# Optimization experiments

Hardware: AMD Instinct MI355X
Metric: run time of the kernel (lower is better)

Reference implementation:

```python
import jax, jax.numpy as jnp
import numpy as np

HIDDEN = 128
N_H = 32
E = 262144


def setup_inputs() -> dict:
    key = jax.random.key(0)
    ks = jax.random.split(key, 10)
    s = lambda fan_in: 1.0 / np.sqrt(fan_in)
    return {
        "h_i": jax.random.normal(ks[0], (E, N_H), dtype=jnp.float32),
        "e_ij": jax.random.normal(ks[1], (E, 1), dtype=jnp.float32),
        # lin_A1: 1 -> HIDDEN
        "W_A1": jax.random.uniform(ks[2], (1, HIDDEN), jnp.float32, -s(1), s(1)),
        "b_A1": jnp.zeros((HIDDEN,), jnp.float32),
        # lin_A2: HIDDEN -> N_H*N_H
        "W_A2": jax.random.uniform(ks[3], (HIDDEN, N_H * N_H), jnp.float32, -s(HIDDEN), s(HIDDEN)),
        "b_A2": jnp.zeros((N_H * N_H,), jnp.float32),
        # lin_b1: 1 -> HIDDEN
        "W_b1": jax.random.uniform(ks[4], (1, HIDDEN), jnp.float32, -s(1), s(1)),
        "b_b1": jnp.zeros((HIDDEN,), jnp.float32),
        # lin_b2: HIDDEN -> N_H
        "W_b2": jax.random.uniform(ks[5], (HIDDEN, N_H), jnp.float32, -s(HIDDEN), s(HIDDEN)),
        "b_b2": jnp.zeros((N_H,), jnp.float32),
    }


def reference(h_i, e_ij, W_A1, b_A1, W_A2, b_A2, W_b1, b_b1, W_b2, b_b2):
    # Per-edge MLP producing an [N_H, N_H] matrix A from the scalar edge feature
    A = jax.nn.selu(e_ij @ W_A1 + b_A1)          # [E, HIDDEN]
    A = (A @ W_A2 + b_A2).reshape(-1, N_H, N_H)  # [E, N_H, N_H]
    # Per-edge MLP producing an [N_H] bias b
    b = jax.nn.selu(e_ij @ W_b1 + b_b1)          # [E, HIDDEN]
    b = b @ W_b2 + b_b2                          # [E, N_H]
    # Batched matvec: m_ij[e, i] = sum_j A[e, i, j] * h_i[e, j] + b[e, i]
    m_ij = jnp.einsum('eij,ej->ei', A, h_i) + b
    return m_ij
```

## Files before the change

kernel.cpp:

```cpp
#include <hip/hip_runtime.h>

#define NH        32
#define HID       128
#define E_TOT     262144
#define CH_ELEM   16384
#define NCH_MAIN  8
#define TAIL_OFF  131072
#define TAIL_ELEM 8192

typedef float        f32x4 __attribute__((ext_vector_type(4)));
typedef short        s16x8 __attribute__((ext_vector_type(8)));
typedef unsigned int u32x4 __attribute__((ext_vector_type(4)));

static __device__ __forceinline__ short f2bf(float f) {
    __bf16 b = (__bf16)f;
    return __builtin_bit_cast(short, b);
}
static __device__ __forceinline__ float selu_f(float x) {
    const float kScale  = 1.0507009873554804934193349852946f;
    const float kAlphaS = 1.7580993408473768599402175208123f;
    float neg = kAlphaS * (__expf(x) - 1.0f);
    return x > 0.0f ? kScale * x : neg;
}

__global__ void wt_build(const float* __restrict__ W_A2, const float* __restrict__ b_A2,
                         const float* __restrict__ W_b2, unsigned short* __restrict__ WT) {
    int gid = blockIdx.x * 256 + threadIdx.x;
    if (gid >= TAIL_OFF + TAIL_ELEM) return;
    int it, g, lrow, p, kap;
    if (gid < TAIL_OFF) {
        int c  = gid >> 14;
        int r  = gid & 16383;
        int sl = r >> 10;
        it   = (r >> 9) & 1;
        g    = (r >> 7) & 3;
        lrow = (r >> 3) & 15;
        p    = r & 7;
        kap  = c * 512 + sl * 32 + g * 8 + p;
    } else {
        int r  = gid - TAIL_OFF;
        int sl = r >> 10;
        it   = (r >> 9) & 1;
        g    = (r >> 7) & 3;
        lrow = (r >> 3) & 15;
        p    = r & 7;
        kap  = 4096 + sl * 32 + g * 8 + p;
    }
    int i = it * 16 + lrow;
    float v = 0.0f;
    if (kap < 4096)      v = W_A2[(kap >> 5) * 1024 + i * 32 + (kap & 31)];
    else if (kap < 4128) v = b_A2[i * 32 + (kap - 4096)];
    else if (kap < 4256) v = W_b2[(kap - 4128) * 32 + i];
    WT[gid] = (unsigned short)f2bf(v);
}

typedef const __attribute__((address_space(1))) unsigned int GU32;
typedef __attribute__((address_space(3))) unsigned int LU32;
static __device__ __forceinline__ void gload_lds16(const void* g, void* l) {
    __builtin_amdgcn_global_load_lds((GU32*)g, (LU32*)l, 16, 0, 0);
}

__global__ void __launch_bounds__(256, 4)
msg_main(const float* __restrict__ h_i, const float* __restrict__ e_ij,
         const float* __restrict__ W_A1, const float* __restrict__ b_A1,
         const float* __restrict__ W_b1, const float* __restrict__ b_b1,
         const float* __restrict__ b_b2,
         const unsigned short* __restrict__ WT,
         float* __restrict__ out)
{
    __shared__ unsigned short ldsW[CH_ELEM];
    __shared__ float cA1[HID], cBA1[HID], cB1a[HID], cB1b[HID], cb2[NH];

    const int tid  = threadIdx.x;
    const int lane = tid & 63;
    const int wid  = tid >> 6;
    const int lrow = lane & 15;
    const int g    = lane >> 4;
    const int e0   = blockIdx.x * 256 + wid * 64;

    if (tid < HID) {
        cA1[tid]  = W_A1[tid];
        cBA1[tid] = b_A1[tid];
        cB1a[tid] = W_b1[tid];
        cB1b[tid] = b_b1[tid];
    }
    if (tid < NH) cb2[tid] = b_b2[tid];

    const float ev_own = e_ij[e0 + lane];

    s16x8 hb[4];
    #pragma unroll
    for (int ct = 0; ct < 4; ++ct) {
        int er = e0 + ct * 16 + lrow;
        const float* hp = h_i + er * 32 + g * 8;
        f32x4 h0 = *(const f32x4*)hp;
        f32x4 h1 = *(const f32x4*)(hp + 4);
        #pragma unroll
        for (int p = 0; p < 4; ++p) {
            hb[ct][p]     = f2bf(h0[p]);
            hb[ct][p + 4] = f2bf(h1[p]);
        }
    }

    float ev_ct[4];
    #pragma unroll
    for (int ct = 0; ct < 4; ++ct) ev_ct[ct] = __shfl(ev_own, ct * 16 + lrow);

    f32x4 acc[4][2];
    #pragma unroll
    for (int ct = 0; ct < 4; ++ct)
        #pragma unroll
        for (int it = 0; it < 2; ++it)
            acc[ct][it] = (f32x4){0.f, 0.f, 0.f, 0.f};
    const f32x4 zf = (f32x4){0.f, 0.f, 0.f, 0.f};

    float u_own[16];

    __syncthreads();

    for (int c = 0; c < NCH_MAIN; ++c) {
        #pragma unroll
        for (int r = 0; r < 8; ++r) {
            int eo = r * 2048 + tid * 8;
            gload_lds16(WT + c * CH_ELEM + eo, &ldsW[eo]);
        }
        #pragma unroll
        for (int sl = 0; sl < 16; ++sl) {
            int s = c * 16 + sl;
            u_own[sl] = selu_f(fmaf(ev_own, cA1[s], cBA1[s]));
        }
        __syncthreads();

        #pragma unroll
        for (int sl = 0; sl < 16; ++sl) {
            u32x4 r0 = *(const u32x4*)&ldsW[sl * 1024 +       lane * 8];
            u32x4 r1 = *(const u32x4*)&ldsW[sl * 1024 + 512 + lane * 8];
            s16x8 A0 = __builtin_bit_cast(s16x8, r0);
            s16x8 A1 = __builtin_bit_cast(s16x8, r1);
            f32x4 u4[4];
            #pragma unroll
            for (int ct = 0; ct < 4; ++ct) {
                float uv = __shfl(u_own[sl], ct * 16 + lrow);
                u4[ct] = (f32x4){uv, uv, uv, uv};
            }
            {
                f32x4 t[4];
                #pragma unroll
                for (int ct = 0; ct < 4; ++ct)
                    t[ct] = __builtin_amdgcn_mfma_f32_16x16x32_bf16(A0, hb[ct], zf, 0, 0, 0);
                #pragma unroll
                for (int ct = 0; ct < 4; ++ct)
                    acc[ct][0] = __builtin_elementwise_fma(t[ct], u4[ct], acc[ct][0]);
            }
            {
                f32x4 t[4];
                #pragma unroll
                for (int ct = 0; ct < 4; ++ct)
                    t[ct] = __builtin_amdgcn_mfma_f32_16x16x32_bf16(A1, hb[ct], zf, 0, 0, 0);
                #pragma unroll
                for (int ct = 0; ct < 4; ++ct)
                    acc[ct][1] = __builtin_elementwise_fma(t[ct], u4[ct], acc[ct][1]);
            }
        }
        __syncthreads();
    }

    #pragma unroll
    for (int r = 0; r < 3; ++r) {
        int eo = r * 2048 + tid * 8;
        gload_lds16(WT + TAIL_OFF + eo, &ldsW[eo]);
    }
    __syncthreads();

    {
        u32x4 r0 = *(const u32x4*)&ldsW[      lane * 8];
        u32x4 r1 = *(const u32x4*)&ldsW[512 + lane * 8];
        s16x8 A0 = __builtin_bit_cast(s16x8, r0);
        s16x8 A1 = __builtin_bit_cast(s16x8, r1);
        #pragma unroll
        for (int ct = 0; ct < 4; ++ct) {
            acc[ct][0] = __builtin_amdgcn_mfma_f32_16x16x32_bf16(A0, hb[ct], acc[ct][0], 0, 0, 0);
            acc[ct][1] = __builtin_amdgcn_mfma_f32_16x16x32_bf16(A1, hb[ct], acc[ct][1], 0, 0, 0);
        }
    }
    #pragma unroll
    for (int q = 0; q < 4; ++q) {
        u32x4 r0 = *(const u32x4*)&ldsW[(q + 1) * 1024 +       lane * 8];
        u32x4 r1 = *(const u32x4*)&ldsW[(q + 1) * 1024 + 512 + lane * 8];
        s16x8 A0 = __builtin_bit_cast(s16x8, r0);
        s16x8 A1 = __builtin_bit_cast(s16x8, r1);
        int tb = q * 32 + g * 8;
        f32x4 wb0 = *(const f32x4*)&cB1a[tb];
        f32x4 wb1 = *(const f32x4*)&cB1a[tb + 4];
        f32x4 bb0 = *(const f32x4*)&cB1b[tb];
        f32x4 bb1 = *(const f32x4*)&cB1b[tb + 4];
        #pragma unroll
        for (int ct = 0; ct < 4; ++ct) {
            s16x8 B;
            #pragma unroll
            for (int p = 0; p < 4; ++p) {
                B[p]     = f2bf(selu_f(fmaf(ev_ct[ct], wb0[p], bb0[p])));
                B[p + 4] = f2bf(selu_f(fmaf(ev_ct[ct], wb1[p], bb1[p])));
            }
            acc[ct][0] = __builtin_amdgcn_mfma_f32_16x16x32_bf16(A0, B, acc[ct][0], 0, 0, 0);
            acc[ct][1] = __builtin_amdgcn_mfma_f32_16x16x32_bf16(A1, B, acc[ct][1], 0, 0, 0);
        }
    }

    #pragma unroll
    for (int it = 0; it < 2; ++it) {
        f32x4 b2v = *(const f32x4*)&cb2[it * 16 + g * 4];
        #pragma unroll
        for (int ct = 0; ct < 4; ++ct) {
            int edge = e0 + ct * 16 + lrow;
            f32x4 vo = acc[ct][it] + b2v;
            *(f32x4*)&out[edge * 32 + it * 16 + g * 4] = vo;
        }
    }
}

extern "C" void kernel_launch(void* const* d_in, const int* in_sizes, int n_in,
                              void* d_out, int out_size, void* d_ws, size_t ws_size,
                              hipStream_t stream) {
    const float* h_i  = (const float*)d_in[0];
    const float* e_ij = (const float*)d_in[1];
    const float* W_A1 = (const float*)d_in[2];
    const float* b_A1 = (const float*)d_in[3];
    const float* W_A2 = (const float*)d_in[4];
    const float* b_A2 = (const float*)d_in[5];
    const float* W_b1 = (const float*)d_in[6];
    const float* b_b1 = (const float*)d_in[7];
    const float* W_b2 = (const float*)d_in[8];
    const float* b_b2 = (const float*)d_in[9];

    unsigned short* WT = (unsigned short*)d_ws;

    wt_build<<<(TAIL_OFF + TAIL_ELEM + 255) / 256, 256, 0, stream>>>(W_A2, b_A2, W_b2, WT);
    msg_main<<<E_TOT / 256, 256, 0, stream>>>(h_i, e_ij, W_A1, b_A1, W_b1, b_b1,
                                              b_b2, WT, (float*)d_out);
}
```

Measured before the change: 97.62 us.

## Split output rows across wave pairs with 512-thread blocks

Each block now runs 8 waves instead of 4. Each pair of waves shares the same 64 edges, and each wave computes one half (16 rows) of the 32-row output. This halves the accumulator registers and MFMA work per wave and raises wave-level parallelism, but each wave now redundantly loads h, computes the selu hidden units and does the b-path selu. The hidden activations are also packed as bf16 pairs, which halves the shuffle count but makes the scale factors coarser than the fp32 values used before.

```diff
diff --git a/kernel.cpp b/kernel.cpp
--- a/kernel.cpp
+++ b/kernel.cpp
@@ -27,12 +27,12 @@
                          const float* __restrict__ W_b2, unsigned short* __restrict__ WT) {
     int gid = blockIdx.x * 256 + threadIdx.x;
     if (gid >= TAIL_OFF + TAIL_ELEM) return;
-    int it, g, lrow, p, kap;
+    int ih, g, lrow, p, kap;
     if (gid < TAIL_OFF) {
         int c  = gid >> 14;
         int r  = gid & 16383;
         int sl = r >> 10;
-        it   = (r >> 9) & 1;
+        ih   = (r >> 9) & 1;
         g    = (r >> 7) & 3;
         lrow = (r >> 3) & 15;
         p    = r & 7;
@@ -40,13 +40,13 @@
     } else {
         int r  = gid - TAIL_OFF;
         int sl = r >> 10;
-        it   = (r >> 9) & 1;
+        ih   = (r >> 9) & 1;
         g    = (r >> 7) & 3;
         lrow = (r >> 3) & 15;
         p    = r & 7;
         kap  = 4096 + sl * 32 + g * 8 + p;
     }
-    int i = it * 16 + lrow;
+    int i = ih * 16 + lrow;
     float v = 0.0f;
     if (kap < 4096)      v = W_A2[(kap >> 5) * 1024 + i * 32 + (kap & 31)];
     else if (kap < 4128) v = b_A2[i * 32 + (kap - 4096)];
@@ -60,7 +60,7 @@
     __builtin_amdgcn_global_load_lds((GU32*)g, (LU32*)l, 16, 0, 0);
 }
 
-__global__ void __launch_bounds__(256, 4)
+__global__ void __launch_bounds__(512, 4)
 msg_main(const float* __restrict__ h_i, const float* __restrict__ e_ij,
          const float* __restrict__ W_A1, const float* __restrict__ b_A1,
          const float* __restrict__ W_b1, const float* __restrict__ b_b1,
@@ -74,9 +74,11 @@
     const int tid  = threadIdx.x;
     const int lane = tid & 63;
     const int wid  = tid >> 6;
+    const int ih   = wid & 1;
+    const int eg   = wid >> 1;
     const int lrow = lane & 15;
     const int g    = lane >> 4;
-    const int e0   = blockIdx.x * 256 + wid * 64;
+    const int e0   = blockIdx.x * 256 + eg * 64;
 
     if (tid < HID) {
         cA1[tid]  = W_A1[tid];
@@ -106,89 +108,80 @@
     #pragma unroll
     for (int ct = 0; ct < 4; ++ct) ev_ct[ct] = __shfl(ev_own, ct * 16 + lrow);
 
-    f32x4 acc[4][2];
-    #pragma unroll
-    for (int ct = 0; ct < 4; ++ct)
-        #pragma unroll
-        for (int it = 0; it < 2; ++it)
-            acc[ct][it] = (f32x4){0.f, 0.f, 0.f, 0.f};
+    f32x4 acc[4];
+    #pragma unroll
+    for (int ct = 0; ct < 4; ++ct) acc[ct] = (f32x4){0.f, 0.f, 0.f, 0.f};
     const f32x4 zf = (f32x4){0.f, 0.f, 0.f, 0.f};
 
-    float u_own[16];
+    unsigned int u_pk[8];
 
     __syncthreads();
 
     for (int c = 0; c < NCH_MAIN; ++c) {
         #pragma unroll
-        for (int r = 0; r < 8; ++r) {
-            int eo = r * 2048 + tid * 8;
+        for (int r = 0; r < 4; ++r) {
+            int eo = r * 4096 + tid * 8;
             gload_lds16(WT + c * CH_ELEM + eo, &ldsW[eo]);
         }
         #pragma unroll
-        for (int sl = 0; sl < 16; ++sl) {
-            int s = c * 16 + sl;
-            u_own[sl] = selu_f(fmaf(ev_own, cA1[s], cBA1[s]));
+        for (int sp = 0; sp < 8; ++sp) {
+            int s = c * 16 + sp * 2;
+            float u0 = selu_f(fmaf(ev_own, cA1[s],     cBA1[s]));
+            float u1 = selu_f(fmaf(ev_own, cA1[s + 1], cBA1[s + 1]));
+            u_pk[sp] = ((unsigned int)(unsigned short)f2bf(u0))
+                     | (((unsigned int)(unsigned short)f2bf(u1)) << 16);
         }
         __syncthreads();
 
         #pragma unroll
-        for (int sl = 0; sl < 16; ++sl) {
-            u32x4 r0 = *(const u32x4*)&ldsW[sl * 1024 +       lane * 8];
-            u32x4 r1 = *(const u32x4*)&ldsW[sl * 1024 + 512 + lane * 8];
-            s16x8 A0 = __builtin_bit_cast(s16x8, r0);
-            s16x8 A1 = __builtin_bit_cast(s16x8, r1);
-            f32x4 u4[4];
+        for (int sp = 0; sp < 8; ++sp) {
+            unsigned int upc[4];
             #pragma unroll
-            for (int ct = 0; ct < 4; ++ct) {
-                float uv = __shfl(u_own[sl], ct * 16 + lrow);
-                u4[ct] = (f32x4){uv, uv, uv, uv};
-            }
-            {
+            for (int ct = 0; ct < 4; ++ct)
+                upc[ct] = __shfl(u_pk[sp], ct * 16 + lrow);
+
+            #pragma unroll
+            for (int half = 0; half < 2; ++half) {
+                const int sl = sp * 2 + half;
+                u32x4 ra = *(const u32x4*)&ldsW[sl * 1024 + ih * 512 + lane * 8];
+                s16x8 A  = __builtin_bit_cast(s16x8, ra);
+                f32x4 u4[4];
+                #pragma unroll
+                for (int ct = 0; ct < 4; ++ct) {
+                    unsigned int w = half == 0 ? (upc[ct] << 16) : (upc[ct] & 0xffff0000u);
+                    float uf = __builtin_bit_cast(float, w);
+                    u4[ct] = (f32x4){uf, uf, uf, uf};
+                }
                 f32x4 t[4];
                 #pragma unroll
                 for (int ct = 0; ct < 4; ++ct)
-                    t[ct] = __builtin_amdgcn_mfma_f32_16x16x32_bf16(A0, hb[ct], zf, 0, 0, 0);
+                    t[ct] = __builtin_amdgcn_mfma_f32_16x16x32_bf16(A, hb[ct], zf, 0, 0, 0);
                 #pragma unroll
                 for (int ct = 0; ct < 4; ++ct)
-                    acc[ct][0] = __builtin_elementwise_fma(t[ct], u4[ct], acc[ct][0]);
+                    acc[ct] = __builtin_elementwise_fma(t[ct], u4[ct], acc[ct]);
             }
-            {
-                f32x4 t[4];
-                #pragma unroll
-                for (int ct = 0; ct < 4; ++ct)
-                    t[ct] = __builtin_amdgcn_mfma_f32_16x16x32_bf16(A1, hb[ct], zf, 0, 0, 0);
-                #pragma unroll
-                for (int ct = 0; ct < 4; ++ct)
-                    acc[ct][1] = __builtin_elementwise_fma(t[ct], u4[ct], acc[ct][1]);
-            }
         }
         __syncthreads();
     }
 
     #pragma unroll
-    for (int r = 0; r < 3; ++r) {
-        int eo = r * 2048 + tid * 8;
+    for (int r = 0; r < 2; ++r) {
+        int eo = r * 4096 + tid * 8;
         gload_lds16(WT + TAIL_OFF + eo, &ldsW[eo]);
     }
     __syncthreads();
 
     {
-        u32x4 r0 = *(const u32x4*)&ldsW[      lane * 8];
-        u32x4 r1 = *(const u32x4*)&ldsW[512 + lane * 8];
-        s16x8 A0 = __builtin_bit_cast(s16x8, r0);
-        s16x8 A1 = __builtin_bit_cast(s16x8, r1);
-        #pragma unroll
-        for (int ct = 0; ct < 4; ++ct) {
-            acc[ct][0] = __builtin_amdgcn_mfma_f32_16x16x32_bf16(A0, hb[ct], acc[ct][0], 0, 0, 0);
-            acc[ct][1] = __builtin_amdgcn_mfma_f32_16x16x32_bf16(A1, hb[ct], acc[ct][1], 0, 0, 0);
-        }
+        u32x4 ra = *(const u32x4*)&ldsW[ih * 512 + lane * 8];
+        s16x8 A  = __builtin_bit_cast(s16x8, ra);
+        #pragma unroll
+        for (int ct = 0; ct < 4; ++ct)
+            acc[ct] = __builtin_amdgcn_mfma_f32_16x16x32_bf16(A, hb[ct], acc[ct], 0, 0, 0);
     }
     #pragma unroll
     for (int q = 0; q < 4; ++q) {
-        u32x4 r0 = *(const u32x4*)&ldsW[(q + 1) * 1024 +       lane * 8];
-        u32x4 r1 = *(const u32x4*)&ldsW[(q + 1) * 1024 + 512 + lane * 8];
-        s16x8 A0 = __builtin_bit_cast(s16x8, r0);
-        s16x8 A1 = __builtin_bit_cast(s16x8, r1);
+        u32x4 ra = *(const u32x4*)&ldsW[(q + 1) * 1024 + ih * 512 + lane * 8];
+        s16x8 A  = __builtin_bit_cast(s16x8, ra);
         int tb = q * 32 + g * 8;
         f32x4 wb0 = *(const f32x4*)&cB1a[tb];
         f32x4 wb1 = *(const f32x4*)&cB1a[tb + 4];
@@ -202,19 +195,17 @@
                 B[p]     = f2bf(selu_f(fmaf(ev_ct[ct], wb0[p], bb0[p])));
                 B[p + 4] = f2bf(selu_f(fmaf(ev_ct[ct], wb1[p], bb1[p])));
             }
-            acc[ct][0] = __builtin_amdgcn_mfma_f32_16x16x32_bf16(A0, B, acc[ct][0], 0, 0, 0);
-            acc[ct][1] = __builtin_amdgcn_mfma_f32_16x16x32_bf16(A1, B, acc[ct][1], 0, 0, 0);
-        }
-    }
-
-    #pragma unroll
-    for (int it = 0; it < 2; ++it) {
-        f32x4 b2v = *(const f32x4*)&cb2[it * 16 + g * 4];
+            acc[ct] = __builtin_amdgcn_mfma_f32_16x16x32_bf16(A, B, acc[ct], 0, 0, 0);
+        }
+    }
+
+    {
+        f32x4 b2v = *(const f32x4*)&cb2[ih * 16 + g * 4];
         #pragma unroll
         for (int ct = 0; ct < 4; ++ct) {
             int edge = e0 + ct * 16 + lrow;
-            f32x4 vo = acc[ct][it] + b2v;
-            *(f32x4*)&out[edge * 32 + it * 16 + g * 4] = vo;
+            f32x4 vo = acc[ct] + b2v;
+            *(f32x4*)&out[edge * 32 + ih * 16 + g * 4] = vo;
         }
     }
 }
@@ -236,6 +227,6 @@
     unsigned short* WT = (unsigned short*)d_ws;
 
     wt_build<<<(TAIL_OFF + TAIL_ELEM + 255) / 256, 256, 0, stream>>>(W_A2, b_A2, W_b2, WT);
-    msg_main<<<E_TOT / 256, 256, 0, stream>>>(h_i, e_ij, W_A1, b_A1, W_b1, b_b1,
+    msg_main<<<E_TOT / 256, 512, 0, stream>>>(h_i, e_ij, W_A1, b_A1, W_b1, b_b1,
                                               b_b2, WT, (float*)d_out);
 }
```

Result: slower. 113.9 us (+16.6%).
